# Kernel optimization log

Measured on AMD Instinct MI355X. Metric: run time of the kernel, lower is better.

## Reference

```python
import jax, jax.numpy as jnp
import numpy as np

B, S, D, H, DK, DFF = 4, 1024, 1024, 16, 64, 4096
EPS = 1e-5


def _layernorm(x, w, b):
    mu = jnp.mean(x, axis=-1, keepdims=True)
    var = jnp.mean((x - mu) ** 2, axis=-1, keepdims=True)
    return (x - mu) / jnp.sqrt(var + EPS) * w + b


def setup_inputs() -> dict:
    root = jax.random.key(0)
    ks = jax.random.split(root, 16)
    g = lambda k, shape, s=0.02: (jax.random.normal(k, shape, dtype=jnp.float32) * s)
    return {
        "mask": 1,
        "query": jax.random.normal(ks[0], (B, S, D), dtype=jnp.float32),
        "key": jax.random.normal(ks[1], (B, S, D), dtype=jnp.float32),
        "values": jax.random.normal(ks[2], (B, S, D), dtype=jnp.float32),
        "Wq": g(ks[3], (D, D)), "bq": jnp.zeros((D,), jnp.float32),
        "Wk": g(ks[4], (D, D)), "bk": jnp.zeros((D,), jnp.float32),
        "Wv": g(ks[5], (D, D)), "bv": jnp.zeros((D,), jnp.float32),
        "Wo": g(ks[6], (D, D)), "bo": jnp.zeros((D,), jnp.float32),
        "gammas": g(ks[7], (H, 1, 1), 0.5),
        "ln1_w": jnp.ones((D,), jnp.float32), "ln1_b": jnp.zeros((D,), jnp.float32),
        "W1": g(ks[8], (DFF, D)), "b1": jnp.zeros((DFF,), jnp.float32),
        "W2": g(ks[9], (D, DFF)), "b2": jnp.zeros((D,), jnp.float32),
        "ln2_w": jnp.ones((D,), jnp.float32), "ln2_b": jnp.zeros((D,), jnp.float32),
    }


def _forward(mask, query, key, values, Wq, bq, Wk, bk, Wv, bv, Wo, bo, gammas,
             ln1_w, ln1_b, W1, b1, W2, b2, ln2_w, ln2_b):
    # mask is a static Python int (the triu offset)
    allowed = jnp.triu(jnp.ones((S, S), dtype=jnp.float32), k=mask) == 0  # [S,S] bool

    def proj(x, W, b):  # [B,S,D] -> [B,H,S,DK]
        return (x @ W.T + b).reshape(B, S, H, DK).transpose(0, 2, 1, 3)

    q = proj(query, Wq, bq)
    k = proj(key, Wk, bk)
    v = proj(values, Wv, bv)

    scores = jnp.einsum('bhid,bhjd->bhij', q, k) / jnp.sqrt(jnp.float32(DK))

    # distance-decay factor, computed without gradient (torch.no_grad + detach)
    def dist_block(sc):
        sc_ = jax.nn.softmax(sc, axis=-1) * allowed.astype(sc.dtype)
        distcum = jnp.cumsum(sc_, axis=-1)
        disttot = jnp.sum(sc_, axis=-1, keepdims=True)
        idx = jnp.arange(S, dtype=jnp.float32)
        pos = jnp.abs(idx[None, :] - idx[:, None])[None, None]  # [1,1,S,S]
        return jnp.sqrt(jnp.clip((disttot - distcum) * pos, 0.0, None))
    dist_scores = jax.lax.stop_gradient(dist_block(scores))

    gamma = -jax.nn.softplus(gammas)[None]  # [1,H,1,1]
    total_effect = jnp.clip(jnp.exp(dist_scores * gamma), 1e-5, 1e5)
    scores = scores * total_effect
    scores = jnp.where(allowed, scores, jnp.float32(-1e20))
    attn = jax.nn.softmax(scores, axis=-1)
    if mask == 0:  # zero_pad first query row
        attn = attn.at[:, :, 0, :].set(0.0)

    out = jnp.einsum('bhij,bhjd->bhid', attn, v)
    concat = out.transpose(0, 2, 1, 3).reshape(B, S, D)
    attn_out = concat @ Wo.T + bo

    x = _layernorm(query + attn_out, ln1_w, ln1_b)
    ffn = jax.nn.relu(x @ W1.T + b1) @ W2.T + b2
    return _layernorm(x + ffn, ln2_w, ln2_b)


def reference(mask, query, key, values, Wq, bq, Wk, bk, Wv, bv, Wo, bo, gammas,
              ln1_w, ln1_b, W1, b1, W2, b2, ln2_w, ln2_b):
    return _forward(mask, query, key, values, Wq, bq, Wk, bk, Wv, bv, Wo, bo,
                    gammas, ln1_w, ln1_b, W1, b1, W2, b2, ln2_w, ln2_b)
```

## Files before the change

### kernel.cpp

```cpp
#include <hip/hip_runtime.h>
#include <hip/hip_bf16.h>
#include <math.h>

#define BB   4
#define SS   1024
#define DDIM 1024
#define HH   16
#define DKK  64
#define DFFF 4096
#define JC2  64

typedef __attribute__((ext_vector_type(8))) short short8;
typedef __attribute__((ext_vector_type(4))) float f32x4;
typedef unsigned short ushort;

__device__ __forceinline__ ushort f2bf(float f) {
    unsigned int u = __float_as_uint(f);
    unsigned int r = (u + 0x7FFFu + ((u >> 16) & 1u)) >> 16;
    return (ushort)r;
}
__device__ __forceinline__ short8 pack8(float4 f0, float4 f1) {
    short8 s;
    s[0] = (short)f2bf(f0.x); s[1] = (short)f2bf(f0.y);
    s[2] = (short)f2bf(f0.z); s[3] = (short)f2bf(f0.w);
    s[4] = (short)f2bf(f1.x); s[5] = (short)f2bf(f1.y);
    s[6] = (short)f2bf(f1.z); s[7] = (short)f2bf(f1.w);
    return s;
}

#define GLD16(g, l) __builtin_amdgcn_global_load_lds( \
    (const __attribute__((address_space(1))) unsigned int*)(g), \
    (__attribute__((address_space(3))) unsigned int*)(l), 16, 0, 0)

__device__ __forceinline__ float fexp2(float x) { return __builtin_amdgcn_exp2f(x); }

__device__ __forceinline__ float scan16(float x) {
    x += __int_as_float(__builtin_amdgcn_update_dpp(0, __float_as_int(x), 0x111, 0xF, 0xF, true));
    x += __int_as_float(__builtin_amdgcn_update_dpp(0, __float_as_int(x), 0x112, 0xF, 0xF, true));
    x += __int_as_float(__builtin_amdgcn_update_dpp(0, __float_as_int(x), 0x114, 0xF, 0xF, true));
    x += __int_as_float(__builtin_amdgcn_update_dpp(0, __float_as_int(x), 0x118, 0xF, 0xF, true));
    return x;
}
__device__ __forceinline__ float bcast15(float x) {
    return __int_as_float(__builtin_amdgcn_ds_swizzle(__float_as_int(x), 0x1F0));
}

__device__ __forceinline__ float block_reduce_sum(float v, float* red, int tid) {
#pragma unroll
    for (int off = 32; off; off >>= 1) v += __shfl_xor(v, off);
    __syncthreads();
    if ((tid & 63) == 0) red[tid >> 6] = v;
    __syncthreads();
    return red[0] + red[1] + red[2] + red[3];
}

struct CvtArgs { const float* s[6]; ushort* d[6]; unsigned int n[6]; };
__global__ __launch_bounds__(256) void convert_bf(CvtArgs a) {
    const int seg = blockIdx.y;
    size_t idx = ((size_t)blockIdx.x * 256 + threadIdx.x) * 8;
    if (idx >= a.n[seg]) return;
    const float* s = a.s[seg];
    float4 f0 = *(const float4*)(s + idx);
    float4 f1 = *(const float4*)(s + idx + 4);
    *(short8*)(a.d[seg] + idx) = pack8(f0, f1);
}

template <int BM, typename TC, bool RELU, bool BIAS, bool CVTA>
__device__ __forceinline__ void gemm_core(const void* __restrict__ Av, int lda,
                                          const ushort* __restrict__ Bm, int ldb,
                                          const float* __restrict__ bias,
                                          TC* __restrict__ C, int N, int Klen,
                                          int bm, int bn) {
    constexpr int MT = BM / 32;
    constexpr int PA = BM / 32;
    __shared__ ushort A_s[BM * 64];
    __shared__ ushort B_s[128 * 64];
    const int t = threadIdx.x;
    const int lane = t & 63, w = t >> 6;
    const int wr = w >> 1, wc = w & 1;
    const int fm = lane & 15, fq = lane >> 4;
    const int srl = lane >> 3;
    const int sg8 = ((lane & 7) ^ srl) << 3;

    f32x4 acc[MT][4];
#pragma unroll
    for (int mt = 0; mt < MT; mt++)
#pragma unroll
        for (int nt = 0; nt < 4; nt++) acc[mt][nt] = (f32x4){0.f, 0.f, 0.f, 0.f};

    for (int kt = 0; kt < Klen; kt += 64) {
        __syncthreads();
        if constexpr (CVTA) {
            const float* Af = (const float*)Av;
#pragma unroll
            for (int p = 0; p < PA; ++p) {
                int rowg = (w * PA + p) * 8;
                const float* src = Af + (size_t)(bm + rowg + srl) * lda + kt + sg8;
                float4 f0 = *(const float4*)(src);
                float4 f1 = *(const float4*)(src + 4);
                *(short8*)&A_s[(rowg + srl) * 64 + ((lane & 7) << 3)] = pack8(f0, f1);
            }
        } else {
            const ushort* A = (const ushort*)Av;
#pragma unroll
            for (int p = 0; p < PA; ++p) {
                int rowg = (w * PA + p) * 8;
                GLD16(A + (size_t)(bm + rowg + srl) * lda + kt + sg8, &A_s[rowg * 64]);
            }
        }
#pragma unroll
        for (int p = 0; p < 4; ++p) {
            int rowg = (w * 4 + p) * 8;
            GLD16(Bm + (size_t)(bn + rowg + srl) * ldb + kt + sg8, &B_s[rowg * 64]);
        }
        __syncthreads();

        short8 av[2][MT], bv[2][4];
        const int sw = fm & 7;
#pragma unroll
        for (int mt = 0; mt < MT; ++mt) {
            int row = wr * (BM / 2) + mt * 16 + fm;
#pragma unroll
            for (int ks = 0; ks < 2; ++ks)
                av[ks][mt] = *(const short8*)&A_s[row * 64 + (((ks * 4 + fq) ^ sw) << 3)];
        }
#pragma unroll
        for (int nt = 0; nt < 4; ++nt) {
            int row = wc * 64 + nt * 16 + fm;
#pragma unroll
            for (int ks = 0; ks < 2; ++ks)
                bv[ks][nt] = *(const short8*)&B_s[row * 64 + (((ks * 4 + fq) ^ sw) << 3)];
        }
#pragma unroll
        for (int ks = 0; ks < 2; ++ks)
#pragma unroll
            for (int mt = 0; mt < MT; ++mt)
#pragma unroll
                for (int nt = 0; nt < 4; ++nt)
                    acc[mt][nt] = __builtin_amdgcn_mfma_f32_16x16x32_bf16(
                        av[ks][mt], bv[ks][nt], acc[mt][nt], 0, 0, 0);
    }

#pragma unroll
    for (int mt = 0; mt < MT; mt++) {
        int row0 = bm + wr * (BM / 2) + mt * 16 + fq * 4;
#pragma unroll
        for (int nt = 0; nt < 4; nt++) {
            int col = bn + wc * 64 + nt * 16 + fm;
            float bsv = BIAS ? bias[col] : 0.f;
#pragma unroll
            for (int r = 0; r < 4; r++) {
                float val = acc[mt][nt][r] + bsv;
                if (RELU) val = fmaxf(val, 0.f);
                if constexpr (sizeof(TC) == 4)
                    ((float*)C)[(size_t)(row0 + r) * N + col] = val;
                else
                    ((ushort*)C)[(size_t)(row0 + r) * N + col] = f2bf(val);
            }
        }
    }
}

template <int BM, typename TC, bool RELU>
__global__ __launch_bounds__(256, 3) void gemm_bf(const ushort* __restrict__ A,
                                                  const ushort* __restrict__ Bm,
                                                  const float* __restrict__ bias,
                                                  TC* __restrict__ C,
                                                  int N, int K) {
    gemm_core<BM, TC, RELU, true, false>(A, K, Bm, K, bias, C, N, K,
                                         blockIdx.y * BM, blockIdx.x * 128);
}

struct QkvArgs { const float* A[3]; const ushort* B[3]; const float* bias[3]; ushort* C[3]; };
__global__ __launch_bounds__(256, 3) void gemm_qkv(QkvArgs qa) {
    const int g = blockIdx.z;
    gemm_core<128, ushort, false, true, true>(qa.A[g], DDIM, qa.B[g], DDIM,
                                              qa.bias[g], qa.C[g], DDIM, DDIM,
                                              blockIdx.y * 128, blockIdx.x * 128);
}

struct SkArgs { const ushort* A; const ushort* Bm; float* C0; float* C1; int lda; int Klen; };
__global__ __launch_bounds__(256, 3) void gemm_splitk(SkArgs s) {
    const int z = blockIdx.z;
    float* C = z ? s.C1 : s.C0;
    const int koff = z * s.Klen;
    gemm_core<128, float, false, false, false>(s.A + koff, s.lda, s.Bm + koff, s.lda,
                                               nullptr, C, DDIM, s.Klen,
                                               blockIdx.y * 128, blockIdx.x * 128);
}

__global__ __launch_bounds__(256, 4) void attn_flash(
    const ushort* __restrict__ Q, const ushort* __restrict__ Kg,
    const ushort* __restrict__ Vg, const float* __restrict__ gammas,
    const int* __restrict__ maskp, ushort* __restrict__ out) {
    __shared__ short QP[64 * 72];
    __shared__ short Ks[JC2 * 72];
    __shared__ short Vts[64 * 72];

    const int t = threadIdx.x;
    const int lane = t & 63, w = t >> 6;
    const int col = lane & 15;
    const int quad = lane >> 4;

    const int bid = blockIdx.x;
    const int xcls = bid & 7;
    const int m = bid >> 3;
    const int bh = xcls + ((m & 7) << 3);
    const int itr = m >> 3;
    const int yy = itr & 3, jj = itr >> 2;
    const int it = (((yy + jj) & 3) << 2) + ((2 * yy + jj) & 3);
    const int h = bh & (HH - 1);
    const int b = bh >> 4;
    const int i0 = it * 64;
    const int mask = *maskp;

    const float LOG2E = 1.44269504f;
    const float SC2 = 0.125f * LOG2E;
    const float g0 = gammas[h];
    const float gnat = -((g0 > 20.f) ? g0 : log1pf(__expf(g0)));
    const float g2 = gnat * LOG2E;

    const size_t qbase = ((size_t)(b * SS + i0)) * DDIM + h * DKK;
    const size_t kvbase = ((size_t)b * SS) * DDIM + h * DKK;

    {
        int r = t >> 2, d0 = (t & 3) << 4;
        const ushort* gq = Q + qbase + (size_t)r * DDIM + d0;
        *(short8*)&QP[r * 72 + d0]     = *(const short8*)(gq);
        *(short8*)&QP[r * 72 + d0 + 8] = *(const short8*)(gq + 8);
    }
    __syncthreads();
    const short8 qa0 = *(const short8*)&QP[(w * 16 + col) * 72 + quad * 8];
    const short8 qa1 = *(const short8*)&QP[(w * 16 + col) * 72 + 32 + quad * 8];

    float m1[4], su[4], smT[4], gi4[4];
    int lim4[4];
#pragma unroll
    for (int r = 0; r < 4; ++r) {
        m1[r] = -3.4e38f; su[r] = 0.f; smT[r] = 0.f;
        int gi = i0 + w * 16 + quad * 4 + r;
        gi4[r] = (float)gi;
        lim4[r] = gi + mask;
    }

    for (int ck = 0; ck < SS / JC2; ++ck) {
        const int jc = ck * JC2;
        __syncthreads();
        {
            int j = t >> 2, d0 = (t & 3) << 4;
            const ushort* gk = Kg + kvbase + (size_t)(jc + j) * DDIM + d0;
            *(short8*)&Ks[j * 72 + d0]     = *(const short8*)(gk);
            *(short8*)&Ks[j * 72 + d0 + 8] = *(const short8*)(gk + 8);
        }
        __syncthreads();
#pragma unroll
        for (int g = 0; g < 4; ++g) {
            short8 kb0 = *(const short8*)&Ks[(g * 16 + col) * 72 + quad * 8];
            short8 kb1 = *(const short8*)&Ks[(g * 16 + col) * 72 + 32 + quad * 8];
            f32x4 c = (f32x4){0.f, 0.f, 0.f, 0.f};
            c = __builtin_amdgcn_mfma_f32_16x16x32_bf16(qa0, kb0, c, 0, 0, 0);
            c = __builtin_amdgcn_mfma_f32_16x16x32_bf16(qa1, kb1, c, 0, 0, 0);
            int j = jc + g * 16 + col;
#pragma unroll
            for (int r = 0; r < 4; ++r) {
                float s2 = c[r] * SC2;
                m1[r] = fmaxf(m1[r], s2);
                float ev = fexp2(s2);
                su[r] += ev;
                smT[r] += (j < lim4[r]) ? ev : 0.f;
            }
        }
    }
#pragma unroll
    for (int off = 1; off < 16; off <<= 1) {
#pragma unroll
        for (int r = 0; r < 4; ++r) {
            m1[r] = fmaxf(m1[r], __shfl_xor(m1[r], off, 16));
            su[r] += __shfl_xor(su[r], off, 16);
            smT[r] += __shfl_xor(smT[r], off, 16);
        }
    }
    float lse2[4], smTn[4], ms2[4];
#pragma unroll
    for (int r = 0; r < 4; ++r) {
        lse2[r] = __log2f(su[r]);
        smTn[r] = smT[r] / su[r];
        ms2[r]  = fmaxf(m1[r], 0.f);
    }

    const int nck2 = min(SS / JC2, max(1, (i0 + 62 + mask) / 64 + 1));

    float l2[4], carry[4];
    f32x4 o[4];
#pragma unroll
    for (int r = 0; r < 4; ++r) { l2[r] = 0.f; carry[r] = 0.f; }
#pragma unroll
    for (int dg = 0; dg < 4; ++dg) o[dg] = (f32x4){0.f, 0.f, 0.f, 0.f};

    short* Pw = &QP[w * 16 * 72];

    for (int ck = 0; ck < nck2; ++ck) {
        const int jc = ck * JC2;
        __syncthreads();
        {
            int j = t >> 2, d0 = (t & 3) << 4;
            const ushort* gk = Kg + kvbase + (size_t)(jc + j) * DDIM + d0;
            *(short8*)&Ks[j * 72 + d0]     = *(const short8*)(gk);
            *(short8*)&Ks[j * 72 + d0 + 8] = *(const short8*)(gk + 8);
        }
        {
            int j = t & 63, dq = t >> 6, d0 = dq * 16;
            const ushort* gv = Vg + kvbase + (size_t)(jc + j) * DDIM + d0;
            short8 v0 = *(const short8*)(gv);
            short8 v1 = *(const short8*)(gv + 8);
#pragma unroll
            for (int k = 0; k < 8; ++k) {
                Vts[(d0 + k) * 72 + j]     = v0[k];
                Vts[(d0 + 8 + k) * 72 + j] = v1[k];
            }
        }
        __syncthreads();

#pragma unroll
        for (int g = 0; g < 4; ++g) {
            short8 kb0 = *(const short8*)&Ks[(g * 16 + col) * 72 + quad * 8];
            short8 kb1 = *(const short8*)&Ks[(g * 16 + col) * 72 + 32 + quad * 8];
            f32x4 c = (f32x4){0.f, 0.f, 0.f, 0.f};
            c = __builtin_amdgcn_mfma_f32_16x16x32_bf16(qa0, kb0, c, 0, 0, 0);
            c = __builtin_amdgcn_mfma_f32_16x16x32_bf16(qa1, kb1, c, 0, 0, 0);
            const int j = jc + g * 16 + col;
            const float jf = (float)j;
#pragma unroll
            for (int r = 0; r < 4; ++r) {
                float s2 = c[r] * SC2;
                float pj = fexp2(s2 - lse2[r]);
                float incl = (j < lim4[r]) ? pj : 0.f;
                incl = scan16(incl);
                float tot = bcast15(incl);
                float Cc = carry[r] + incl;
                carry[r] += tot;
                float pos = fabsf(jf - gi4[r]);
                float d2 = fmaxf((smTn[r] - Cc) * pos, 0.f);
                float dist = __builtin_amdgcn_sqrtf(d2);
                float eff = fmaxf(fexp2(g2 * dist), 1e-5f);
                float pe = fexp2(s2 * eff - ms2[r]);
                float p = (j < lim4[r]) ? pe : 0.f;
                l2[r] += p;
                Pw[(quad * 4 + r) * 72 + g * 16 + col] = (short)f2bf(p);
            }
        }
        __syncthreads();
#pragma unroll
        for (int kg = 0; kg < 2; ++kg) {
            short8 pa = *(const short8*)&Pw[col * 72 + kg * 32 + quad * 8];
#pragma unroll
            for (int dg = 0; dg < 4; ++dg) {
                short8 vb = *(const short8*)&Vts[(dg * 16 + col) * 72 + kg * 32 + quad * 8];
                o[dg] = __builtin_amdgcn_mfma_f32_16x16x32_bf16(pa, vb, o[dg], 0, 0, 0);
            }
        }
    }

#pragma unroll
    for (int off = 1; off < 16; off <<= 1)
#pragma unroll
        for (int r = 0; r < 4; ++r) l2[r] += __shfl_xor(l2[r], off, 16);

#pragma unroll
    for (int r = 0; r < 4; ++r) {
        int irow = i0 + w * 16 + quad * 4 + r;
        float scl = 1.f / l2[r];
        if (mask == 0 && irow == 0) scl = 0.f;
        size_t base = ((size_t)(b * SS) + irow) * DDIM + h * DKK;
#pragma unroll
        for (int dg = 0; dg < 4; ++dg)
            out[base + dg * 16 + col] = f2bf(o[dg][r] * scl);
    }
}

template <bool WB>
__global__ __launch_bounds__(256) void add_ln(const float* __restrict__ R,
                                              const float* __restrict__ Y0,
                                              const float* __restrict__ Y1,
                                              const float* __restrict__ gb,
                                              const float* __restrict__ w,
                                              const float* __restrict__ bb,
                                              float* __restrict__ out,
                                              ushort* __restrict__ obf) {
    const int row = blockIdx.x;
    const int tid = threadIdx.x;
    __shared__ float red[4];
    __shared__ float xs[DDIM];
    const size_t base = (size_t)row * DDIM;
    float s = 0.f, s2 = 0.f;
#pragma unroll
    for (int l = 0; l < 4; l++) {
        int idx = tid + l * 256;
        float x = R[base + idx] + Y0[base + idx] + Y1[base + idx] + gb[idx];
        xs[idx] = x;
        s += x;
        s2 += x * x;
    }
    s = block_reduce_sum(s, red, tid);
    s2 = block_reduce_sum(s2, red, tid);
    const float mu = s * (1.f / DDIM);
    const float var = s2 * (1.f / DDIM) - mu * mu;
    const float rstd = rsqrtf(var + 1e-5f);
#pragma unroll
    for (int l = 0; l < 4; l++) {
        int idx = tid + l * 256;
        float v = (xs[idx] - mu) * rstd * w[idx] + bb[idx];
        out[base + idx] = v;
        if (WB) obf[base + idx] = f2bf(v);
    }
}

extern "C" void kernel_launch(void* const* d_in, const int* in_sizes, int n_in,
                              void* d_out, int out_size, void* d_ws, size_t ws_size,
                              hipStream_t stream) {
    const int*   maskp  = (const int*)d_in[0];
    const float* query  = (const float*)d_in[1];
    const float* key    = (const float*)d_in[2];
    const float* values = (const float*)d_in[3];
    const float* Wq = (const float*)d_in[4];
    const float* bq = (const float*)d_in[5];
    const float* Wk = (const float*)d_in[6];
    const float* bk = (const float*)d_in[7];
    const float* Wv = (const float*)d_in[8];
    const float* bv = (const float*)d_in[9];
    const float* Wo = (const float*)d_in[10];
    const float* bo = (const float*)d_in[11];
    const float* gammas = (const float*)d_in[12];
    const float* ln1w = (const float*)d_in[13];
    const float* ln1b = (const float*)d_in[14];
    const float* W1 = (const float*)d_in[15];
    const float* b1 = (const float*)d_in[16];
    const float* W2 = (const float*)d_in[17];
    const float* b2 = (const float*)d_in[18];
    const float* ln2w = (const float*)d_in[19];
    const float* ln2b = (const float*)d_in[20];

    const int M = BB * SS;
    const size_t MB = 1048576;
    char* wsb = (char*)d_ws;
    ushort* Wq_bf = (ushort*)(wsb + 0 * MB);
    ushort* Wk_bf = (ushort*)(wsb + 8 * MB);
    ushort* Wv_bf = (ushort*)(wsb + 16 * MB);
    ushort* Wo_bf = (ushort*)(wsb + 24 * MB);
    ushort* W1_bf = (ushort*)(wsb + 32 * MB);
    ushort* W2_bf = (ushort*)(wsb + 40 * MB);
    ushort* Qb    = (ushort*)(wsb + 72 * MB);
    ushort* Kb    = (ushort*)(wsb + 80 * MB);
    ushort* Vb    = (ushort*)(wsb + 88 * MB);
    ushort* ATTb  = (ushort*)(wsb + 96 * MB);
    float*  Ysp0  = (float*)(wsb + 104 * MB);
    float*  Ysp1  = (float*)(wsb + 120 * MB);
    float*  xf    = (float*)(wsb + 48 * MB);
    ushort* x_bf  = (ushort*)(wsb + 64 * MB);
    ushort* hidden= (ushort*)(wsb + 72 * MB);

    dim3 blk(256);

    const unsigned int N4M = 4u * 1024 * 1024, N1M = 1024 * 1024;
    CvtArgs ca;
    ca.s[0] = Wq; ca.s[1] = Wk; ca.s[2] = Wv; ca.s[3] = Wo;
    ca.s[4] = W1; ca.s[5] = W2;
    ca.d[0] = Wq_bf; ca.d[1] = Wk_bf; ca.d[2] = Wv_bf; ca.d[3] = Wo_bf;
    ca.d[4] = W1_bf; ca.d[5] = W2_bf;
    ca.n[0] = N1M; ca.n[1] = N1M; ca.n[2] = N1M; ca.n[3] = N1M;
    ca.n[4] = N4M; ca.n[5] = N4M;
    convert_bf<<<dim3(2048, 6), blk, 0, stream>>>(ca);

    QkvArgs qa;
    qa.A[0] = query; qa.A[1] = key; qa.A[2] = values;
    qa.B[0] = Wq_bf; qa.B[1] = Wk_bf; qa.B[2] = Wv_bf;
    qa.bias[0] = bq; qa.bias[1] = bk; qa.bias[2] = bv;
    qa.C[0] = Qb; qa.C[1] = Kb; qa.C[2] = Vb;
    gemm_qkv<<<dim3(8, 32, 3), blk, 0, stream>>>(qa);

    attn_flash<<<dim3(BB * HH * 16), blk, 0, stream>>>(Qb, Kb, Vb, gammas, maskp, ATTb);

    {
        SkArgs s; s.A = ATTb; s.Bm = Wo_bf; s.C0 = Ysp0; s.C1 = Ysp1;
        s.lda = DDIM; s.Klen = DDIM / 2;
        gemm_splitk<<<dim3(8, 32, 2), blk, 0, stream>>>(s);
    }

    add_ln<true><<<dim3(M), blk, 0, stream>>>(query, Ysp0, Ysp1, bo, ln1w, ln1b, xf, x_bf);

    gemm_bf<128, ushort, true><<<dim3(32, 32), blk, 0, stream>>>(x_bf, W1_bf, b1, hidden, DFFF, DDIM);

    {
        SkArgs s; s.A = hidden; s.Bm = W2_bf; s.C0 = Ysp0; s.C1 = Ysp1;
        s.lda = DFFF; s.Klen = DFFF / 2;
        gemm_splitk<<<dim3(8, 32, 2), blk, 0, stream>>>(s);
    }

    add_ln<false><<<dim3(M), blk, 0, stream>>>(xf, Ysp0, Ysp1, b2, ln2w, ln2b, (float*)d_out, nullptr);
}
```

Measured before the change: 419.0 us.

## Double-buffer swizzled K tiles in attention with async global-to-LDS loads

The attention kernel now stages K chunks into two XOR-swizzled LDS buffers with direct global-to-LDS loads (GLD16), prefetching the next chunk while the current one is consumed. This drops one barrier per iteration in both passes. The last prefetch of the stats pass wraps around to load chunk 0, so the second pass starts with its first K tile already resident. Separately, the GEMM kernels' launch bounds drop from 3 to 2 waves per SIMD, allowing more registers at the cost of occupancy. Correctness depends on the async loads being complete before the end-of-iteration barrier, and on the reduced barrier count still protecting Vts and Pw reuse.

```diff
diff --git a/kernel.cpp b/kernel.cpp
--- a/kernel.cpp
+++ b/kernel.cpp
@@ -162,7 +162,7 @@
 }
 
 template <int BM, typename TC, bool RELU>
-__global__ __launch_bounds__(256, 3) void gemm_bf(const ushort* __restrict__ A,
+__global__ __launch_bounds__(256, 2) void gemm_bf(const ushort* __restrict__ A,
                                                   const ushort* __restrict__ Bm,
                                                   const float* __restrict__ bias,
                                                   TC* __restrict__ C,
@@ -172,7 +172,7 @@
 }
 
 struct QkvArgs { const float* A[3]; const ushort* B[3]; const float* bias[3]; ushort* C[3]; };
-__global__ __launch_bounds__(256, 3) void gemm_qkv(QkvArgs qa) {
+__global__ __launch_bounds__(256, 2) void gemm_qkv(QkvArgs qa) {
     const int g = blockIdx.z;
     gemm_core<128, ushort, false, true, true>(qa.A[g], DDIM, qa.B[g], DDIM,
                                               qa.bias[g], qa.C[g], DDIM, DDIM,
@@ -180,7 +180,7 @@
 }
 
 struct SkArgs { const ushort* A; const ushort* Bm; float* C0; float* C1; int lda; int Klen; };
-__global__ __launch_bounds__(256, 3) void gemm_splitk(SkArgs s) {
+__global__ __launch_bounds__(256, 2) void gemm_splitk(SkArgs s) {
     const int z = blockIdx.z;
     float* C = z ? s.C1 : s.C0;
     const int koff = z * s.Klen;
@@ -194,13 +194,16 @@
     const ushort* __restrict__ Vg, const float* __restrict__ gammas,
     const int* __restrict__ maskp, ushort* __restrict__ out) {
     __shared__ short QP[64 * 72];
-    __shared__ short Ks[JC2 * 72];
+    __shared__ short KsD[2][64 * 64];
     __shared__ short Vts[64 * 72];
 
     const int t = threadIdx.x;
     const int lane = t & 63, w = t >> 6;
     const int col = lane & 15;
     const int quad = lane >> 4;
+    const int srl = lane >> 3;
+    const int sg8 = ((lane & 7) ^ srl) << 3;
+    const int swk = col & 7;
 
     const int bid = blockIdx.x;
     const int xcls = bid & 7;
@@ -223,11 +226,18 @@
     const size_t qbase = ((size_t)(b * SS + i0)) * DDIM + h * DKK;
     const size_t kvbase = ((size_t)b * SS) * DDIM + h * DKK;
 
+#define STAGE_K(jc, kb) \
+    { _Pragma("unroll") for (int p = 0; p < 2; ++p) { \
+        int rowg = (w * 2 + p) * 8; \
+        GLD16(Kg + kvbase + (size_t)((jc) + rowg + srl) * DDIM + sg8, \
+              &KsD[kb][rowg * 64]); } }
+
     {
         int r = t >> 2, d0 = (t & 3) << 4;
         const ushort* gq = Q + qbase + (size_t)r * DDIM + d0;
         *(short8*)&QP[r * 72 + d0]     = *(const short8*)(gq);
         *(short8*)&QP[r * 72 + d0 + 8] = *(const short8*)(gq + 8);
+        STAGE_K(0, 0);
     }
     __syncthreads();
     const short8 qa0 = *(const short8*)&QP[(w * 16 + col) * 72 + quad * 8];
@@ -243,20 +253,16 @@
         lim4[r] = gi + mask;
     }
 
+    int buf = 0;
     for (int ck = 0; ck < SS / JC2; ++ck) {
         const int jc = ck * JC2;
-        __syncthreads();
-        {
-            int j = t >> 2, d0 = (t & 3) << 4;
-            const ushort* gk = Kg + kvbase + (size_t)(jc + j) * DDIM + d0;
-            *(short8*)&Ks[j * 72 + d0]     = *(const short8*)(gk);
-            *(short8*)&Ks[j * 72 + d0 + 8] = *(const short8*)(gk + 8);
-        }
-        __syncthreads();
+        const int njc = ((ck + 1) & 15) * JC2;
+        STAGE_K(njc, buf ^ 1);
 #pragma unroll
         for (int g = 0; g < 4; ++g) {
-            short8 kb0 = *(const short8*)&Ks[(g * 16 + col) * 72 + quad * 8];
-            short8 kb1 = *(const short8*)&Ks[(g * 16 + col) * 72 + 32 + quad * 8];
+            const short* Kr = &KsD[buf][(g * 16 + col) * 64];
+            short8 kb0 = *(const short8*)&Kr[(quad ^ swk) << 3];
+            short8 kb1 = *(const short8*)&Kr[((4 + quad) ^ swk) << 3];
             f32x4 c = (f32x4){0.f, 0.f, 0.f, 0.f};
             c = __builtin_amdgcn_mfma_f32_16x16x32_bf16(qa0, kb0, c, 0, 0, 0);
             c = __builtin_amdgcn_mfma_f32_16x16x32_bf16(qa1, kb1, c, 0, 0, 0);
@@ -270,6 +276,8 @@
                 smT[r] += (j < lim4[r]) ? ev : 0.f;
             }
         }
+        __syncthreads();
+        buf ^= 1;
     }
 #pragma unroll
     for (int off = 1; off < 16; off <<= 1) {
@@ -301,13 +309,7 @@
 
     for (int ck = 0; ck < nck2; ++ck) {
         const int jc = ck * JC2;
-        __syncthreads();
-        {
-            int j = t >> 2, d0 = (t & 3) << 4;
-            const ushort* gk = Kg + kvbase + (size_t)(jc + j) * DDIM + d0;
-            *(short8*)&Ks[j * 72 + d0]     = *(const short8*)(gk);
-            *(short8*)&Ks[j * 72 + d0 + 8] = *(const short8*)(gk + 8);
-        }
+        if (ck + 1 < nck2) STAGE_K((ck + 1) * JC2, buf ^ 1);
         {
             int j = t & 63, dq = t >> 6, d0 = dq * 16;
             const ushort* gv = Vg + kvbase + (size_t)(jc + j) * DDIM + d0;
@@ -319,12 +321,12 @@
                 Vts[(d0 + 8 + k) * 72 + j] = v1[k];
             }
         }
-        __syncthreads();
 
 #pragma unroll
         for (int g = 0; g < 4; ++g) {
-            short8 kb0 = *(const short8*)&Ks[(g * 16 + col) * 72 + quad * 8];
-            short8 kb1 = *(const short8*)&Ks[(g * 16 + col) * 72 + 32 + quad * 8];
+            const short* Kr = &KsD[buf][(g * 16 + col) * 64];
+            short8 kb0 = *(const short8*)&Kr[(quad ^ swk) << 3];
+            short8 kb1 = *(const short8*)&Kr[((4 + quad) ^ swk) << 3];
             f32x4 c = (f32x4){0.f, 0.f, 0.f, 0.f};
             c = __builtin_amdgcn_mfma_f32_16x16x32_bf16(qa0, kb0, c, 0, 0, 0);
             c = __builtin_amdgcn_mfma_f32_16x16x32_bf16(qa1, kb1, c, 0, 0, 0);
@@ -359,6 +361,8 @@
                 o[dg] = __builtin_amdgcn_mfma_f32_16x16x32_bf16(pa, vb, o[dg], 0, 0, 0);
             }
         }
+        __syncthreads();
+        buf ^= 1;
     }
 
 #pragma unroll
@@ -376,6 +380,7 @@
         for (int dg = 0; dg < 4; ++dg)
             out[base + dg * 16 + col] = f2bf(o[dg][r] * scl);
     }
+#undef STAGE_K
 }
 
 template <bool WB>
```

Result: faster. 400.7 us (-4.4%).
